# Kernel tuning notes

Hardware: AMD Instinct MI355X
Metric: run time of the kernel (lower is better)

The kernel has to match this reference:

```python
import jax, jax.numpy as jnp
import numpy as np

B, S, H = 64, 512, 768
A1, C1 = 100, 300          # token-attention and sentence-classifier hidden sizes
BETA = 1.0                 # soft_attention_beta
SLW, TLW, RLW = 1.0, 1.0, 0.01  # loss weights


def setup_inputs() -> dict:
    key = jax.random.key(0)
    ks = jax.random.split(key, 12)
    hidden_states = jax.random.normal(ks[0], (B, S, H), jnp.float32)
    # token_attention: Linear(H,100) -> Tanh -> Linear(100,1) -> Sigmoid
    w1 = jax.random.normal(ks[1], (H, A1), jnp.float32) * 0.02
    b1 = jnp.zeros((A1,), jnp.float32)
    w2 = jax.random.normal(ks[2], (A1, 1), jnp.float32) * 0.02
    b2 = jnp.zeros((1,), jnp.float32)
    # sentence_classification: Linear(H,300) -> Tanh -> Linear(300,1) -> Sigmoid
    sw1 = jax.random.normal(ks[3], (H, C1), jnp.float32) * 0.02
    sb1 = jnp.zeros((C1,), jnp.float32)
    sw2 = jax.random.normal(ks[4], (C1, 1), jnp.float32) * 0.02
    sb2 = jnp.zeros((1,), jnp.float32)
    offset_mapping = jax.random.randint(ks[5], (B, S, 2), 0, 4).astype(jnp.int32)
    offset_mapping = offset_mapping.at[:, 0, 0].set(0)  # first token starts a word
    # labels in {-1, 0, 1}; -1 = ignore
    labels = jax.random.randint(ks[6], (B, S), -1, 2).astype(jnp.float32)
    return {
        "hidden_states": hidden_states,
        "w1": w1, "b1": b1, "w2": w2, "b2": b2,
        "sw1": sw1, "sb1": sb1, "sw2": sw2, "sb2": sb2,
        "labels": labels,
        "offset_mapping": offset_mapping,
    }


def _forward(hidden_states, w1, b1, w2, b2, sw1, sb1, sw2, sb2, labels, offset_mapping):
    # token attention scores in (0,1): [B, S]
    token_att = jax.nn.sigmoid(
        jnp.tanh(hidden_states @ w1 + b1) @ w2 + b2
    )[..., 0]

    # ragged per-word subword max-pooling (segment-max along the sequence)
    not_subword = offset_mapping[:, :, 0] == 0                 # [B, S] word starts
    seg = jnp.maximum(jnp.cumsum(not_subword.astype(jnp.int32), axis=1) - 1, 0)

    def _seg_max(vals, seg_ids):
        return jax.ops.segment_max(vals, seg_ids, num_segments=S)

    segmax = jax.vmap(_seg_max)(token_att, seg)                # [B, S] per-word max
    word_att = jnp.where(not_subword, jnp.take_along_axis(segmax, seg, axis=1), 0.0)

    # mask: labeled tokens that are word starts
    token_mask = ((labels != -1) & not_subword).astype(token_att.dtype)
    masked = word_att * token_mask                              # token_logits [B, S]

    # beta-normalized soft attention pooling over hidden states
    p = masked ** BETA
    att_norm = p / jnp.sum(p, axis=1, keepdims=True)            # [B, S]
    pooled = jnp.einsum("bsh,bs->bh", hidden_states, att_norm)  # [B, H]

    sent = jax.nn.sigmoid(jnp.tanh(pooled @ sw1 + sb1) @ sw2 + sb2)  # [B, 1]

    # losses (MSE with reduction='sum')
    sentence_labels = jnp.max(labels, axis=1, keepdims=True)    # [B, 1]
    sentence_loss = jnp.sum((sent - sentence_labels) ** 2)
    zero_labels = jnp.where(labels != -1, labels, 0.0)
    token_loss = jnp.sum((masked - zero_labels) ** 2)
    ones_masked = jnp.where(masked == 0, 1.0, masked)
    reg_a = jnp.sum(jnp.min(ones_masked, axis=1, keepdims=True) ** 2)
    reg_b = jnp.sum((jnp.max(masked, axis=1, keepdims=True) - sentence_labels) ** 2)
    total = SLW * sentence_loss + TLW * token_loss + RLW * (reg_a + reg_b)
    return total, sentence_loss, token_loss, reg_a, reg_b, masked, sent


def reference(hidden_states, w1, b1, w2, b2, sw1, sb1, sw2, sb2, labels, offset_mapping):
    return _forward(hidden_states, w1, b1, w2, b2, sw1, sb1, sw2, sb2,
                    labels, offset_mapping)
```

## Files before the change

### kernel.cpp

```cpp
#include <hip/hip_runtime.h>
#include <math.h>

#define BB 64
#define SS 512
#define HH 768
#define AA1 100
#define CC1 300

typedef __bf16 bf16x8 __attribute__((ext_vector_type(8)));
typedef float f32x4 __attribute__((ext_vector_type(4)));

#ifndef __has_builtin
#define __has_builtin(x) 0
#endif
#if __has_builtin(__builtin_amdgcn_global_load_lds)
#define HAVE_GLL 1
#else
#define HAVE_GLL 0
#endif

#define AS1 __attribute__((address_space(1)))
#define AS3 __attribute__((address_space(3)))

__global__ __launch_bounds__(256) void k_prep(const float* __restrict__ w1,
                                              __bf16* __restrict__ w1i) {
    int idx = blockIdx.x * 256 + threadIdx.x;
    int j = idx % 112;
    int r = idx / 112;
    int e = r & 7, g = r >> 3;
    int k = (g >> 2) * 32 + (g & 3) * 8 + e;
    float v = (j < AA1) ? w1[k * AA1 + j] : 0.f;
    w1i[((size_t)g * 112 + j) * 8 + e] = (__bf16)v;
}

__global__ __launch_bounds__(256) void k_token_att(
        const float* __restrict__ hs, const __bf16* __restrict__ w1i,
        const float* __restrict__ b1, const float* __restrict__ w2,
        const float* __restrict__ b2, float* __restrict__ token_att) {
    __shared__ __attribute__((aligned(16))) float lA[2048];
    __shared__ __attribute__((aligned(16))) __bf16 lB[3584];

    const int tid = threadIdx.x;
    const int tok0 = blockIdx.x * 64;
    const int w = tid >> 6, lane = tid & 63;
    const int q = lane >> 4, ln = lane & 15;
    const int t = w * 16 + ln;

    f32x4 acc[7];
#pragma unroll
    for (int n = 0; n < 7; n++) acc[n] = (f32x4){0.f, 0.f, 0.f, 0.f};

    const int p0 = (2 * q) ^ (ln & 7);
    const int p1 = (2 * q + 1) ^ (ln & 7);

    for (int kt = 0; kt < 24; kt++) {
        const int ko = kt * 32;
        {
            int i0 = tid;
            int t0 = i0 >> 3, c0 = (i0 & 7) ^ (t0 & 7);
            const float* g0 = hs + (size_t)(tok0 + t0) * HH + ko + c0 * 4;
            int i1 = tid + 256;
            int t1 = i1 >> 3, c1 = (i1 & 7) ^ (t1 & 7);
            const float* g1 = hs + (size_t)(tok0 + t1) * HH + ko + c1 * 4;
            const __bf16* gb0 = w1i + (size_t)kt * 3584 + (size_t)tid * 8;
#if HAVE_GLL
            __builtin_amdgcn_global_load_lds((AS1 void*)g0,
                    (AS3 void*)(lA + (w * 64) * 4), 16, 0, 0);
            __builtin_amdgcn_global_load_lds((AS1 void*)g1,
                    (AS3 void*)(lA + (256 + w * 64) * 4), 16, 0, 0);
            __builtin_amdgcn_global_load_lds((AS1 void*)gb0,
                    (AS3 void*)(lB + (w * 64) * 8), 16, 0, 0);
            if (w < 3) {
                const __bf16* gb1 = w1i + (size_t)kt * 3584 + (size_t)(tid + 256) * 8;
                __builtin_amdgcn_global_load_lds((AS1 void*)gb1,
                        (AS3 void*)(lB + (256 + w * 64) * 8), 16, 0, 0);
            }
#else
            *(f32x4*)&lA[i0 * 4] = *(const f32x4*)g0;
            *(f32x4*)&lA[i1 * 4] = *(const f32x4*)g1;
            *(bf16x8*)&lB[(size_t)tid * 8] = *(const bf16x8*)gb0;
            if (tid < 192) {
                const __bf16* gb1 = w1i + (size_t)kt * 3584 + (size_t)(tid + 256) * 8;
                *(bf16x8*)&lB[(size_t)(tid + 256) * 8] = *(const bf16x8*)gb1;
            }
#endif
        }
        __syncthreads();
        f32x4 a0 = *(f32x4*)&lA[(t * 8 + p0) * 4];
        f32x4 a1 = *(f32x4*)&lA[(t * 8 + p1) * 4];
        bf16x8 af;
        af[0] = (__bf16)a0[0]; af[1] = (__bf16)a0[1];
        af[2] = (__bf16)a0[2]; af[3] = (__bf16)a0[3];
        af[4] = (__bf16)a1[0]; af[5] = (__bf16)a1[1];
        af[6] = (__bf16)a1[2]; af[7] = (__bf16)a1[3];
#pragma unroll
        for (int n = 0; n < 7; n++) {
            bf16x8 bf = *(bf16x8*)&lB[((size_t)q * 112 + n * 16 + ln) * 8];
            acc[n] = __builtin_amdgcn_mfma_f32_16x16x32_bf16(af, bf, acc[n], 0, 0, 0);
        }
        __syncthreads();
    }

    float s0 = 0.f, s1 = 0.f, s2 = 0.f, s3 = 0.f;
#pragma unroll
    for (int n = 0; n < 7; n++) {
        int j = n * 16 + ln;
        if (j < AA1) {
            float bj = b1[j], wj = w2[j];
            s0 += tanhf(acc[n][0] + bj) * wj;
            s1 += tanhf(acc[n][1] + bj) * wj;
            s2 += tanhf(acc[n][2] + bj) * wj;
            s3 += tanhf(acc[n][3] + bj) * wj;
        }
    }
#pragma unroll
    for (int off = 1; off < 16; off <<= 1) {
        s0 += __shfl_xor(s0, off);
        s1 += __shfl_xor(s1, off);
        s2 += __shfl_xor(s2, off);
        s3 += __shfl_xor(s3, off);
    }
    if (ln == 0) {
        float bb = b2[0];
        int base = tok0 + w * 16 + q * 4;
        token_att[base + 0] = 1.f / (1.f + expf(-(s0 + bb)));
        token_att[base + 1] = 1.f / (1.f + expf(-(s1 + bb)));
        token_att[base + 2] = 1.f / (1.f + expf(-(s2 + bb)));
        token_att[base + 3] = 1.f / (1.f + expf(-(s3 + bb)));
    }
}

__global__ __launch_bounds__(512) void k_tail(
        const float* __restrict__ hs, const float* __restrict__ token_att,
        const float* __restrict__ labels, const int* __restrict__ offm,
        const float* __restrict__ sw1, const float* __restrict__ sb1,
        const float* __restrict__ sw2, const float* __restrict__ sb2,
        float* __restrict__ masked_out, float* __restrict__ sent_out,
        float* __restrict__ out) {
    __shared__ int smax[512];
    __shared__ int wscan[8];
    __shared__ int wscan2[8];
    __shared__ float wred[5][8];
    __shared__ float cw[512];
    __shared__ short cs[512];
    __shared__ float pool[HH];
    __shared__ float wsum[8];

    const int b = blockIdx.x, s = threadIdx.x;
    const int lane = s & 63, wv = s >> 6;
    const int ns = (offm[(b * SS + s) * 2] == 0) ? 1 : 0;

    int v = ns;
#pragma unroll
    for (int off = 1; off < 64; off <<= 1) {
        int o = __shfl_up(v, off);
        if (lane >= off) v += o;
    }
    if (lane == 63) wscan[wv] = v;
    smax[s] = 0;
    __syncthreads();
    int woff = 0;
    for (int i = 0; i < 8; i++) woff += (i < wv) ? wscan[i] : 0;
    const int seg = max(v + woff - 1, 0);

    const float ta = token_att[b * SS + s];
    atomicMax(&smax[seg], __float_as_int(ta));
    __syncthreads();

    const float wa = ns ? __int_as_float(smax[seg]) : 0.f;
    const float lab = labels[b * SS + s];
    const float m = (lab != -1.f && ns) ? wa : 0.f;
    masked_out[b * SS + s] = m;

    const float zl = (lab != -1.f) ? lab : 0.f;
    const float tl = (m - zl) * (m - zl);
    const float ones = (m == 0.f) ? 1.f : m;

    float r0 = m, r1 = tl, r2 = m, r3 = ones, r4 = lab;
#pragma unroll
    for (int off = 32; off > 0; off >>= 1) {
        r0 += __shfl_xor(r0, off);
        r1 += __shfl_xor(r1, off);
        r2 = fmaxf(r2, __shfl_xor(r2, off));
        r3 = fminf(r3, __shfl_xor(r3, off));
        r4 = fmaxf(r4, __shfl_xor(r4, off));
    }
    if (lane == 0) {
        wred[0][wv] = r0; wred[1][wv] = r1; wred[2][wv] = r2;
        wred[3][wv] = r3; wred[4][wv] = r4;
    }

    const int nz = (m != 0.f) ? 1 : 0;
    int v2 = nz;
#pragma unroll
    for (int off = 1; off < 64; off <<= 1) {
        int o = __shfl_up(v2, off);
        if (lane >= off) v2 += o;
    }
    if (lane == 63) wscan2[wv] = v2;
    __syncthreads();

    float att = 0.f, tokl = 0.f, maxm = -1e30f, minone = 1e30f, slab = -1e30f;
    for (int i = 0; i < 8; i++) {
        att += wred[0][i]; tokl += wred[1][i];
        maxm = fmaxf(maxm, wred[2][i]);
        minone = fminf(minone, wred[3][i]);
        slab = fmaxf(slab, wred[4][i]);
    }
    int woff2 = 0, nnz = 0;
    for (int i = 0; i < 8; i++) {
        woff2 += (i < wv) ? wscan2[i] : 0;
        nnz += wscan2[i];
    }
    if (nz) {
        int pos = v2 + woff2 - 1;
        cw[pos] = m;
        cs[pos] = (short)s;
    }
    __syncthreads();

    const float inv = 1.f / att;
    float a0 = 0.f, a1 = 0.f;
    const float* hsb = hs + (size_t)b * SS * HH;
    for (int i = 0; i < nnz; i++) {
        const float wv_ = cw[i];
        const float* hp = hsb + (size_t)cs[i] * HH;
        a0 += hp[s] * wv_;
        if (s < 256) a1 += hp[s + 512] * wv_;
    }
    pool[s] = a0 * inv;
    if (s < 256) pool[s + 512] = a1 * inv;
    __syncthreads();

    float tt = 0.f;
    if (s < CC1) {
        float z = sb1[s];
#pragma unroll 8
        for (int k = 0; k < HH; k++) z += pool[k] * sw1[k * CC1 + s];
        tt = tanhf(z) * sw2[s];
    }
#pragma unroll
    for (int off = 32; off > 0; off >>= 1) tt += __shfl_xor(tt, off);
    if (lane == 0) wsum[wv] = tt;
    __syncthreads();

    if (s == 0) {
        float zsum = 0.f;
        for (int i = 0; i < 8; i++) zsum += wsum[i];
        float sv = 1.f / (1.f + expf(-(zsum + sb2[0])));
        sent_out[b] = sv;
        float vs = sv - slab; vs *= vs;
        float ra = minone * minone;
        float rb = maxm - slab; rb *= rb;
        atomicAdd(&out[1], vs);
        atomicAdd(&out[2], tokl);
        atomicAdd(&out[3], ra);
        atomicAdd(&out[4], rb);
        atomicAdd(&out[0], vs + tokl + 0.01f * (ra + rb));
    }
}

extern "C" void kernel_launch(void* const* d_in, const int* in_sizes, int n_in,
                              void* d_out, int out_size, void* d_ws, size_t ws_size,
                              hipStream_t stream) {
    const float* hs  = (const float*)d_in[0];
    const float* w1  = (const float*)d_in[1];
    const float* b1  = (const float*)d_in[2];
    const float* w2  = (const float*)d_in[3];
    const float* b2  = (const float*)d_in[4];
    const float* sw1 = (const float*)d_in[5];
    const float* sb1 = (const float*)d_in[6];
    const float* sw2 = (const float*)d_in[7];
    const float* sb2 = (const float*)d_in[8];
    const float* labels = (const float*)d_in[9];
    const int*   offm   = (const int*)d_in[10];

    float* out = (float*)d_out;
    float* ws  = (float*)d_ws;

    float*  token_att = ws;
    __bf16* w1i       = (__bf16*)(ws + 32768);

    float* masked_out = out + 5;
    float* sent_out   = out + 5 + BB * SS;

    hipMemsetAsync(out, 0, 5 * sizeof(float), stream);
    hipLaunchKernelGGL(k_prep, dim3(336), dim3(256), 0, stream, w1, w1i);
    hipLaunchKernelGGL(k_token_att, dim3(512), dim3(256), 0, stream,
                       hs, w1i, b1, w2, b2, token_att);
    hipLaunchKernelGGL(k_tail, dim3(BB), dim3(512), 0, stream,
                       hs, token_att, labels, offm, sw1, sb1, sw2, sb2,
                       masked_out, sent_out, out);
}
```

Baseline: 258.7 us.

## Split tail kernel into mask, parallel pooling, and sentence-classifier kernels

The single per-batch tail kernel is split into three kernels: a mask/statistics kernel that writes compacted nonzero weights and indices to workspace, a pooling kernel gridded over batch and three hidden-dimension chunks with eight independent accumulators for memory-level parallelism, and a final sentence-classifier kernel. This aims to raise parallelism and load concurrency in the gather-weighted pooling, which previously ran on only 64 blocks with a serial dependent accumulation. In exchange it adds two kernel launches and global-memory round trips for the intermediates.

```diff
diff --git a/kernel.cpp b/kernel.cpp
--- a/kernel.cpp
+++ b/kernel.cpp
@@ -130,21 +130,16 @@
     }
 }
 
-__global__ __launch_bounds__(512) void k_tail(
-        const float* __restrict__ hs, const float* __restrict__ token_att,
-        const float* __restrict__ labels, const int* __restrict__ offm,
-        const float* __restrict__ sw1, const float* __restrict__ sb1,
-        const float* __restrict__ sw2, const float* __restrict__ sb2,
-        float* __restrict__ masked_out, float* __restrict__ sent_out,
-        float* __restrict__ out) {
+__global__ __launch_bounds__(512) void k_mask(
+        const float* __restrict__ token_att, const float* __restrict__ labels,
+        const int* __restrict__ offm, float* __restrict__ masked_out,
+        float* __restrict__ cw_g, short* __restrict__ cs_g,
+        int* __restrict__ nnz_g, float* __restrict__ inv_g,
+        float4* __restrict__ stats_g) {
     __shared__ int smax[512];
     __shared__ int wscan[8];
     __shared__ int wscan2[8];
     __shared__ float wred[5][8];
-    __shared__ float cw[512];
-    __shared__ short cs[512];
-    __shared__ float pool[HH];
-    __shared__ float wsum[8];
 
     const int b = blockIdx.x, s = threadIdx.x;
     const int lane = s & 63, wv = s >> 6;
@@ -200,63 +195,98 @@
     if (lane == 63) wscan2[wv] = v2;
     __syncthreads();
 
-    float att = 0.f, tokl = 0.f, maxm = -1e30f, minone = 1e30f, slab = -1e30f;
-    for (int i = 0; i < 8; i++) {
-        att += wred[0][i]; tokl += wred[1][i];
-        maxm = fmaxf(maxm, wred[2][i]);
-        minone = fminf(minone, wred[3][i]);
-        slab = fmaxf(slab, wred[4][i]);
-    }
-    int woff2 = 0, nnz = 0;
-    for (int i = 0; i < 8; i++) {
-        woff2 += (i < wv) ? wscan2[i] : 0;
-        nnz += wscan2[i];
-    }
+    int woff2 = 0;
+    for (int i = 0; i < 8; i++) woff2 += (i < wv) ? wscan2[i] : 0;
     if (nz) {
         int pos = v2 + woff2 - 1;
-        cw[pos] = m;
-        cs[pos] = (short)s;
-    }
-    __syncthreads();
-
-    const float inv = 1.f / att;
-    float a0 = 0.f, a1 = 0.f;
-    const float* hsb = hs + (size_t)b * SS * HH;
-    for (int i = 0; i < nnz; i++) {
-        const float wv_ = cw[i];
-        const float* hp = hsb + (size_t)cs[i] * HH;
-        a0 += hp[s] * wv_;
-        if (s < 256) a1 += hp[s + 512] * wv_;
-    }
-    pool[s] = a0 * inv;
-    if (s < 256) pool[s + 512] = a1 * inv;
+        cw_g[b * SS + pos] = m;
+        cs_g[b * SS + pos] = (short)s;
+    }
+    if (s == 0) {
+        float att = 0.f, tokl = 0.f, maxm = -1e30f, minone = 1e30f, slab = -1e30f;
+        int nnz = 0;
+        for (int i = 0; i < 8; i++) {
+            att += wred[0][i]; tokl += wred[1][i];
+            maxm = fmaxf(maxm, wred[2][i]);
+            minone = fminf(minone, wred[3][i]);
+            slab = fmaxf(slab, wred[4][i]);
+            nnz += wscan2[i];
+        }
+        nnz_g[b] = nnz;
+        inv_g[b] = 1.f / att;
+        stats_g[b] = make_float4(tokl, maxm, minone, slab);
+    }
+}
+
+__global__ __launch_bounds__(256) void k_pool(
+        const float* __restrict__ hs, const float* __restrict__ cw_g,
+        const short* __restrict__ cs_g, const int* __restrict__ nnz_g,
+        const float* __restrict__ inv_g, float* __restrict__ pooled) {
+    __shared__ float w[SS];
+    __shared__ short idx[SS];
+    const int b = blockIdx.x, g = blockIdx.y, tid = threadIdx.x;
+    const int nnz = nnz_g[b];
+    for (int i = tid; i < nnz; i += 256) {
+        w[i] = cw_g[b * SS + i];
+        idx[i] = cs_g[b * SS + i];
+    }
+    __syncthreads();
+    const int h = g * 256 + tid;
+    const float* hsb = hs + (size_t)b * SS * HH + h;
+    float a0 = 0.f, a1 = 0.f, a2 = 0.f, a3 = 0.f;
+    float a4 = 0.f, a5 = 0.f, a6 = 0.f, a7 = 0.f;
+    int i = 0;
+    for (; i + 8 <= nnz; i += 8) {
+        a0 += hsb[(size_t)idx[i + 0] * HH] * w[i + 0];
+        a1 += hsb[(size_t)idx[i + 1] * HH] * w[i + 1];
+        a2 += hsb[(size_t)idx[i + 2] * HH] * w[i + 2];
+        a3 += hsb[(size_t)idx[i + 3] * HH] * w[i + 3];
+        a4 += hsb[(size_t)idx[i + 4] * HH] * w[i + 4];
+        a5 += hsb[(size_t)idx[i + 5] * HH] * w[i + 5];
+        a6 += hsb[(size_t)idx[i + 6] * HH] * w[i + 6];
+        a7 += hsb[(size_t)idx[i + 7] * HH] * w[i + 7];
+    }
+    for (; i < nnz; i++) a0 += hsb[(size_t)idx[i] * HH] * w[i];
+    float acc = ((a0 + a1) + (a2 + a3)) + ((a4 + a5) + (a6 + a7));
+    pooled[b * HH + h] = acc * inv_g[b];
+}
+
+__global__ __launch_bounds__(320) void k_sentfinal(
+        const float* __restrict__ pooled, const float4* __restrict__ stats_g,
+        const float* __restrict__ sw1, const float* __restrict__ sb1,
+        const float* __restrict__ sw2, const float* __restrict__ sb2,
+        float* __restrict__ sent_out, float* __restrict__ out) {
+    __shared__ float p[HH];
+    __shared__ float wsum[5];
+    const int b = blockIdx.x, tid = threadIdx.x;
+    const int lane = tid & 63, wv = tid >> 6;
+    for (int i = tid; i < HH; i += 320) p[i] = pooled[b * HH + i];
     __syncthreads();
 
     float tt = 0.f;
-    if (s < CC1) {
-        float z = sb1[s];
+    if (tid < CC1) {
+        float z = sb1[tid];
 #pragma unroll 8
-        for (int k = 0; k < HH; k++) z += pool[k] * sw1[k * CC1 + s];
-        tt = tanhf(z) * sw2[s];
+        for (int k = 0; k < HH; k++) z += p[k] * sw1[k * CC1 + tid];
+        tt = tanhf(z) * sw2[tid];
     }
 #pragma unroll
     for (int off = 32; off > 0; off >>= 1) tt += __shfl_xor(tt, off);
     if (lane == 0) wsum[wv] = tt;
     __syncthreads();
-
-    if (s == 0) {
-        float zsum = 0.f;
-        for (int i = 0; i < 8; i++) zsum += wsum[i];
+    if (tid == 0) {
+        float zsum = wsum[0] + wsum[1] + wsum[2] + wsum[3] + wsum[4];
         float sv = 1.f / (1.f + expf(-(zsum + sb2[0])));
         sent_out[b] = sv;
-        float vs = sv - slab; vs *= vs;
-        float ra = minone * minone;
-        float rb = maxm - slab; rb *= rb;
+        float4 st = stats_g[b];
+        float vs = sv - st.w; vs *= vs;
+        float ra = st.z * st.z;
+        float rb = st.y - st.w; rb *= rb;
         atomicAdd(&out[1], vs);
-        atomicAdd(&out[2], tokl);
+        atomicAdd(&out[2], st.x);
         atomicAdd(&out[3], ra);
         atomicAdd(&out[4], rb);
-        atomicAdd(&out[0], vs + tokl + 0.01f * (ra + rb));
+        atomicAdd(&out[0], vs + st.x + 0.01f * (ra + rb));
     }
 }
 
@@ -279,7 +309,13 @@
     float* ws  = (float*)d_ws;
 
     float*  token_att = ws;
-    __bf16* w1i       = (__bf16*)(ws + 32768);
+    __bf16* w1i    = (__bf16*)(ws + 32768);
+    float*  cw     = ws + 32768 + 43008;
+    short*  cs     = (short*)(cw + 32768);
+    int*    nnz    = (int*)(cw + 32768 + 16384);
+    float*  inv    = (float*)(nnz + 64);
+    float4* stats  = (float4*)(inv + 64);
+    float*  pooled = inv + 64 + 256;
 
     float* masked_out = out + 5;
     float* sent_out   = out + 5 + BB * SS;
@@ -288,7 +324,11 @@
     hipLaunchKernelGGL(k_prep, dim3(336), dim3(256), 0, stream, w1, w1i);
     hipLaunchKernelGGL(k_token_att, dim3(512), dim3(256), 0, stream,
                        hs, w1i, b1, w2, b2, token_att);
-    hipLaunchKernelGGL(k_tail, dim3(BB), dim3(512), 0, stream,
-                       hs, token_att, labels, offm, sw1, sb1, sw2, sb2,
-                       masked_out, sent_out, out);
-}
+    hipLaunchKernelGGL(k_mask, dim3(BB), dim3(512), 0, stream,
+                       token_att, labels, offm, masked_out,
+                       cw, cs, nnz, inv, stats);
+    hipLaunchKernelGGL(k_pool, dim3(BB, 3), dim3(256), 0, stream,
+                       hs, cw, cs, nnz, inv, pooled);
+    hipLaunchKernelGGL(k_sentfinal, dim3(BB), dim3(320), 0, stream,
+                       pooled, stats, sw1, sb1, sw2, sb2, sent_out, out);
+}
```

Measured after the change: 246.9 us. 1.05x faster.
